# Performance work log

Measured on AMD Instinct MI355X. Metric: run time of the kernel, lower is better.

## Reference

```python
import jax, jax.numpy as jnp
import numpy as np

N_NODES = 50000
N_EDGES = 600000
D = 128
HIDDEN = 128
N_GRAPHS = 128
N_CLASSES = 10
N_STACKED = 3  # num_layers - 1


def setup_inputs() -> dict:
    key = jax.random.key(0)
    ks = jax.random.split(key, 12)
    s = 1.0 / np.sqrt(HIDDEN)
    inp = {
        "x": jax.random.normal(ks[0], (N_NODES, D), dtype=jnp.float32),
        "edge_index": jax.random.randint(ks[1], (2, N_EDGES), 0, N_NODES, dtype=jnp.int64),
        "batch": jnp.sort(jax.random.randint(ks[2], (N_NODES,), 0, N_GRAPHS, dtype=jnp.int64)),
        "W1": jax.random.normal(ks[3], (D, HIDDEN), dtype=jnp.float32) * s,
        "R1": jax.random.normal(ks[4], (D, HIDDEN), dtype=jnp.float32) * s,
        "b1": jnp.zeros((HIDDEN,), dtype=jnp.float32),
        "Wc": jax.random.normal(ks[5], (N_STACKED, HIDDEN, HIDDEN), dtype=jnp.float32) * s,
        "Rc": jax.random.normal(ks[6], (N_STACKED, HIDDEN, HIDDEN), dtype=jnp.float32) * s,
        "bc": jnp.zeros((N_STACKED, HIDDEN), dtype=jnp.float32),
        "lin1_w": jax.random.normal(ks[7], (HIDDEN, HIDDEN), dtype=jnp.float32) * s,
        "lin1_b": jnp.zeros((HIDDEN,), dtype=jnp.float32),
        "lin2_w": jax.random.normal(ks[8], (HIDDEN, N_CLASSES), dtype=jnp.float32) * s,
        "lin2_b": jnp.zeros((N_CLASSES,), dtype=jnp.float32),
    }
    return inp


def _gcn_norm(edge_index, n_nodes):
    # symmetric GCN normalization coeffs per edge (edge_weight=None -> ones)
    src, dst = edge_index[0], edge_index[1]
    ones = jnp.ones((edge_index.shape[1],), dtype=jnp.float32)
    deg = jax.ops.segment_sum(ones, dst, num_segments=n_nodes)
    dinv = jnp.where(deg > 0, jax.lax.rsqrt(jnp.maximum(deg, 1.0)), 0.0)
    return dinv[src] * dinv[dst]


def _gcs(x, src, dst, norm, W, R, b):
    # GCN aggregation on transformed features + linear skip (root) connection
    h = x @ W                                   # [N, H]
    msg = h[src] * norm[:, None]                # gather + scale, [E, H]
    agg = jax.ops.segment_sum(msg, dst, num_segments=x.shape[0])
    return agg + x @ R + b


def reference(x, edge_index, batch, W1, R1, b1, Wc, Rc, bc,
              lin1_w, lin1_b, lin2_w, lin2_b):
    src, dst = edge_index[0], edge_index[1]
    norm = _gcn_norm(edge_index, x.shape[0])

    h = jax.nn.relu(_gcs(x, src, dst, norm, W1, R1, b1))
    for i in range(N_STACKED):
        h = jax.nn.relu(_gcs(h, src, dst, norm, Wc[i], Rc[i], bc[i]))
    last = h

    # global mean pool over graphs
    sums = jax.ops.segment_sum(h, batch, num_segments=N_GRAPHS)
    cnts = jax.ops.segment_sum(jnp.ones((h.shape[0],), h.dtype), batch,
                               num_segments=N_GRAPHS)
    pooled = sums / jnp.maximum(cnts, 1.0)[:, None]

    g = jax.nn.relu(pooled @ lin1_w + lin1_b)   # dropout is identity in eval mode
    logits = g @ lin2_w + lin2_b
    return jax.nn.log_softmax(logits, axis=-1), last
```

## Files before the change

kernel.cpp:

```cpp
#include <hip/hip_runtime.h>

#define N_NODES  50000
#define N_EDGES  600000
#define DIM      128
#define N_GRAPHS 128
#define N_CLASSES 10
#define NB_SCAN  196
#define ZWORDS   1700000
#define NZB4     1661


typedef __bf16 bf16x8 __attribute__((ext_vector_type(8)));
typedef float  f32x4  __attribute__((ext_vector_type(4)));

__device__ inline unsigned short f2bf(float f) {
  union { float f; unsigned int i; } u; u.f = f;
  unsigned int r = u.i + 0x7fff + ((u.i >> 16) & 1);
  return (unsigned short)(r >> 16);
}
__device__ inline float bf2f(unsigned short s) {
  union { unsigned int i; float f; } u; u.i = ((unsigned int)s) << 16;
  return u.f;
}
__device__ inline bf16x8 pack8(float4 lo, float4 hi) {
  union { bf16x8 v; unsigned short s[8]; } u;
  u.s[0] = f2bf(lo.x); u.s[1] = f2bf(lo.y); u.s[2] = f2bf(lo.z); u.s[3] = f2bf(lo.w);
  u.s[4] = f2bf(hi.x); u.s[5] = f2bf(hi.y); u.s[6] = f2bf(hi.z); u.s[7] = f2bf(hi.w);
  return u.v;
}
__device__ inline bf16x8 zero8() {
  union { bf16x8 v; unsigned short s[8]; } u;
#pragma unroll
  for (int j = 0; j < 8; ++j) u.s[j] = 0;
  return u.v;
}


__global__ __launch_bounds__(256) void k_prep(float4* __restrict__ z4,
                                              const float* __restrict__ W1,
                                              const float* __restrict__ R1,
                                              const float* __restrict__ Wc,
                                              const float* __restrict__ Rc,
                                              unsigned short* __restrict__ pk) {
  if (blockIdx.x < NZB4) {
    int i = blockIdx.x * 256 + threadIdx.x;
    if (i < ZWORDS / 4) z4[i] = make_float4(0.f, 0.f, 0.f, 0.f);
    return;
  }
  int pb = blockIdx.x - NZB4;
  int mm = pb >> 3, sub = pb & 7;
  const float* src = (mm == 0) ? W1
                   : (mm < 4)  ? Wc + (size_t)(mm - 1) * DIM * DIM
                   : (mm == 4) ? R1
                               : Rc + (size_t)(mm - 5) * DIM * DIM;
  int idx = sub * 256 + threadIdx.x;
  int lane = idx & 63;
  int kc   = (idx >> 6) & 3;
  int nt   = idx >> 8;
  int col  = nt * 16 + (lane & 15);
  int k0   = kc * 32 + (lane >> 4) * 8;
  unsigned short* dst = pk + (size_t)mm * 16384 + (size_t)idx * 8;
  ushort4 u;
  u.x = f2bf(src[(k0 + 0) * DIM + col]);
  u.y = f2bf(src[(k0 + 1) * DIM + col]);
  u.z = f2bf(src[(k0 + 2) * DIM + col]);
  u.w = f2bf(src[(k0 + 3) * DIM + col]);
  *(ushort4*)&dst[0] = u;
  u.x = f2bf(src[(k0 + 4) * DIM + col]);
  u.y = f2bf(src[(k0 + 5) * DIM + col]);
  u.z = f2bf(src[(k0 + 6) * DIM + col]);
  u.w = f2bf(src[(k0 + 7) * DIM + col]);
  *(ushort4*)&dst[4] = u;
}


__global__ __launch_bounds__(256) void k_deg(const int* __restrict__ ei,
                                             int* __restrict__ deg) {
  int e = blockIdx.x * 256 + threadIdx.x;
  if (e < N_EDGES) atomicAdd(&deg[ei[N_EDGES + e]], 1);
}

__global__ __launch_bounds__(256) void k_dinvsum(const int* __restrict__ deg,
                                                 float* __restrict__ dinv,
                                                 int* __restrict__ bsum) {
  int i = blockIdx.x * 256 + threadIdx.x;
  int t = threadIdx.x;
  int d = (i < N_NODES) ? deg[i] : 0;
  if (i < N_NODES) dinv[i] = (d > 0) ? rsqrtf((float)d) : 0.f;
  int dp = (d + 7) & ~7;
  __shared__ int tmp[256];
  tmp[t] = dp;
  __syncthreads();
  for (int off = 128; off > 0; off >>= 1) {
    if (t < off) tmp[t] += tmp[t + off];
    __syncthreads();
  }
  if (t == 0) bsum[blockIdx.x] = tmp[0];
}

__global__ __launch_bounds__(256) void k_bscan(const int* __restrict__ bsum,
                                               int* __restrict__ boff,
                                               int* __restrict__ rowp) {
  int t = threadIdx.x;
  int v = (t < NB_SCAN) ? bsum[t] : 0;
  __shared__ int tmp[256];
  tmp[t] = v;
  __syncthreads();
  for (int off = 1; off < 256; off <<= 1) {
    int add = (t >= off) ? tmp[t - off] : 0;
    __syncthreads();
    tmp[t] += add;
    __syncthreads();
  }
  boff[t] = tmp[t] - v;
  if (t == 255) rowp[N_NODES] = tmp[255];
}

__global__ __launch_bounds__(256) void k_rowp(const int* __restrict__ deg,
                                              const int* __restrict__ boff,
                                              int* __restrict__ rowp) {
  int i = blockIdx.x * 256 + threadIdx.x;
  int t = threadIdx.x;
  int dp = (i < N_NODES) ? ((deg[i] + 7) & ~7) : 0;
  __shared__ int tmp[256];
  tmp[t] = dp;
  __syncthreads();
  for (int off = 1; off < 256; off <<= 1) {
    int add = (t >= off) ? tmp[t - off] : 0;
    __syncthreads();
    tmp[t] += add;
    __syncthreads();
  }
  if (i < N_NODES) rowp[i] = boff[blockIdx.x] + tmp[t] - dp;
}

__global__ __launch_bounds__(256) void k_fill(const int* __restrict__ ei,
                                              const int* __restrict__ rowp,
                                              int* __restrict__ cnt,
                                              const float* __restrict__ dinv,
                                              int2* __restrict__ epk) {
  int e = blockIdx.x * 256 + threadIdx.x;
  if (e < N_EDGES) {
    int s = ei[e];
    int d = ei[N_EDGES + e];
    int p = rowp[d] + atomicAdd(&cnt[d], 1);
    epk[p] = make_int2(s, __float_as_int(dinv[s] * dinv[d]));
  }
}


__global__ __launch_bounds__(256) void k_gemm0(const float* __restrict__ xf,
                                               const unsigned short* __restrict__ pkW,
                                               const unsigned short* __restrict__ pkR,
                                               const float* __restrict__ bv,
                                               unsigned short* __restrict__ hwb,
                                               unsigned short* __restrict__ skipb) {
  const int tid  = threadIdx.x;
  const int wave = tid >> 6, lane = tid & 63;
  const int m = lane & 15, q = lane >> 4;
  const int rbase = blockIdx.x * 64 + wave * 16;
  const int arow  = rbase + m;
  const bool aok  = arow < N_NODES;

  bf16x8 a[4];
#pragma unroll
  for (int kc = 0; kc < 4; ++kc) {
    float4 lo = make_float4(0.f, 0.f, 0.f, 0.f);
    float4 hi = make_float4(0.f, 0.f, 0.f, 0.f);
    if (aok) {
      lo = *(const float4*)&xf[arow * DIM + kc * 32 + q * 8];
      hi = *(const float4*)&xf[arow * DIM + kc * 32 + q * 8 + 4];
    }
    a[kc] = pack8(lo, hi);
  }

  f32x4 acc[16];
#pragma unroll
  for (int t = 0; t < 16; ++t) acc[t] = (f32x4){0.f, 0.f, 0.f, 0.f};

#pragma unroll
  for (int nt = 0; nt < 8; ++nt) {
    const unsigned short* pw = pkW + ((size_t)(nt * 4) * 64 + lane) * 8;
    const unsigned short* pr = pkR + ((size_t)(nt * 4) * 64 + lane) * 8;
#pragma unroll
    for (int kc = 0; kc < 4; ++kc) {
      bf16x8 bW = *(const bf16x8*)(pw + (size_t)kc * 64 * 8);
      acc[nt] = __builtin_amdgcn_mfma_f32_16x16x32_bf16(a[kc], bW, acc[nt], 0, 0, 0);
    }
#pragma unroll
    for (int kc = 0; kc < 4; ++kc) {
      bf16x8 bR = *(const bf16x8*)(pr + (size_t)kc * 64 * 8);
      acc[8 + nt] = __builtin_amdgcn_mfma_f32_16x16x32_bf16(a[kc], bR, acc[8 + nt], 0, 0, 0);
    }
  }

#pragma unroll
  for (int nt = 0; nt < 8; ++nt) {
    int col = nt * 16 + m;
    float bias = bv[col];
#pragma unroll
    for (int rg = 0; rg < 4; ++rg) {
      int row = rbase + q * 4 + rg;
      if (row < N_NODES) {
        hwb[row * DIM + col]   = f2bf(acc[nt][rg]);
        skipb[row * DIM + col] = f2bf(acc[8 + nt][rg] + bias);
      }
    }
  }
}


__global__ __launch_bounds__(256) void k_gath(const unsigned short* __restrict__ hin,
                                              const int* __restrict__ rowp,
                                              const int2* __restrict__ epk,
                                              const unsigned short* __restrict__ skipb,
                                              unsigned short* __restrict__ gout) {
  int n = blockIdx.x * 8 + (threadIdx.x >> 5);
  if (n >= N_NODES) return;
  int l4 = (threadIdx.x & 31) * 4;
  int e0 = rowp[n], e1 = rowp[n + 1];
  ushort4 s = *(const ushort4*)&skipb[n * DIM + l4];
  float4 accA = make_float4(0.f, 0.f, 0.f, 0.f);
  float4 accB = make_float4(0.f, 0.f, 0.f, 0.f);
  for (int ea = e0, eb = e1 - 4; ea < eb; ea += 4, eb -= 4) {
    int4 p0 = *(const int4*)&epk[ea];
    int4 p1 = *(const int4*)&epk[ea + 2];
    int4 p2 = *(const int4*)&epk[eb];
    int4 p3 = *(const int4*)&epk[eb + 2];
    ushort4 u0 = *(const ushort4*)&hin[p0.x * DIM + l4];
    ushort4 u1 = *(const ushort4*)&hin[p0.z * DIM + l4];
    ushort4 u2 = *(const ushort4*)&hin[p1.x * DIM + l4];
    ushort4 u3 = *(const ushort4*)&hin[p1.z * DIM + l4];
    ushort4 u4 = *(const ushort4*)&hin[p2.x * DIM + l4];
    ushort4 u5 = *(const ushort4*)&hin[p2.z * DIM + l4];
    ushort4 u6 = *(const ushort4*)&hin[p3.x * DIM + l4];
    ushort4 u7 = *(const ushort4*)&hin[p3.z * DIM + l4];
    float w0 = __int_as_float(p0.y), w1 = __int_as_float(p0.w);
    float w2 = __int_as_float(p1.y), w3 = __int_as_float(p1.w);
    float w4 = __int_as_float(p2.y), w5 = __int_as_float(p2.w);
    float w6 = __int_as_float(p3.y), w7 = __int_as_float(p3.w);
    accA.x = fmaf(w0, bf2f(u0.x), fmaf(w1, bf2f(u1.x), fmaf(w2, bf2f(u2.x), fmaf(w3, bf2f(u3.x), accA.x))));
    accA.y = fmaf(w0, bf2f(u0.y), fmaf(w1, bf2f(u1.y), fmaf(w2, bf2f(u2.y), fmaf(w3, bf2f(u3.y), accA.y))));
    accA.z = fmaf(w0, bf2f(u0.z), fmaf(w1, bf2f(u1.z), fmaf(w2, bf2f(u2.z), fmaf(w3, bf2f(u3.z), accA.z))));
    accA.w = fmaf(w0, bf2f(u0.w), fmaf(w1, bf2f(u1.w), fmaf(w2, bf2f(u2.w), fmaf(w3, bf2f(u3.w), accA.w))));
    accB.x = fmaf(w4, bf2f(u4.x), fmaf(w5, bf2f(u5.x), fmaf(w6, bf2f(u6.x), fmaf(w7, bf2f(u7.x), accB.x))));
    accB.y = fmaf(w4, bf2f(u4.y), fmaf(w5, bf2f(u5.y), fmaf(w6, bf2f(u6.y), fmaf(w7, bf2f(u7.y), accB.y))));
    accB.z = fmaf(w4, bf2f(u4.z), fmaf(w5, bf2f(u5.z), fmaf(w6, bf2f(u6.z), fmaf(w7, bf2f(u7.z), accB.z))));
    accB.w = fmaf(w4, bf2f(u4.w), fmaf(w5, bf2f(u5.w), fmaf(w6, bf2f(u6.w), fmaf(w7, bf2f(u7.w), accB.w))));
  }
  ushort4 o;
  o.x = f2bf(fmaxf(accA.x + accB.x + bf2f(s.x), 0.f));
  o.y = f2bf(fmaxf(accA.y + accB.y + bf2f(s.y), 0.f));
  o.z = f2bf(fmaxf(accA.z + accB.z + bf2f(s.z), 0.f));
  o.w = f2bf(fmaxf(accA.w + accB.w + bf2f(s.w), 0.f));
  *(ushort4*)&gout[n * DIM + l4] = o;
}


template<bool LAST>
__global__ __launch_bounds__(256) void k_gemmb(unsigned short* __restrict__ gio,
                                               const unsigned short* __restrict__ pkW,
                                               const unsigned short* __restrict__ pkR,
                                               const float* __restrict__ bv,
                                               unsigned short* __restrict__ skipb,
                                               float* __restrict__ skipf) {
  const int tid  = threadIdx.x;
  const int wave = tid >> 6, lane = tid & 63;
  const int m = lane & 15, q = lane >> 4;
  const int rbase = blockIdx.x * 64 + wave * 16;
  const int arow  = rbase + m;
  const bool aok  = arow < N_NODES;

  bf16x8 a[4];
#pragma unroll
  for (int kc = 0; kc < 4; ++kc)
    a[kc] = aok ? *(const bf16x8*)&gio[arow * DIM + kc * 32 + q * 8] : zero8();

  f32x4 acc[16];
#pragma unroll
  for (int t = 0; t < 16; ++t) acc[t] = (f32x4){0.f, 0.f, 0.f, 0.f};

#pragma unroll
  for (int nt = 0; nt < 8; ++nt) {
    const unsigned short* pw = pkW + ((size_t)(nt * 4) * 64 + lane) * 8;
    const unsigned short* pr = pkR + ((size_t)(nt * 4) * 64 + lane) * 8;
#pragma unroll
    for (int kc = 0; kc < 4; ++kc) {
      bf16x8 bW = *(const bf16x8*)(pw + (size_t)kc * 64 * 8);
      acc[nt] = __builtin_amdgcn_mfma_f32_16x16x32_bf16(a[kc], bW, acc[nt], 0, 0, 0);
    }
#pragma unroll
    for (int kc = 0; kc < 4; ++kc) {
      bf16x8 bR = *(const bf16x8*)(pr + (size_t)kc * 64 * 8);
      acc[8 + nt] = __builtin_amdgcn_mfma_f32_16x16x32_bf16(a[kc], bR, acc[8 + nt], 0, 0, 0);
    }
  }

#pragma unroll
  for (int nt = 0; nt < 8; ++nt) {
    int col = nt * 16 + m;
    float bias = bv[col];
#pragma unroll
    for (int rg = 0; rg < 4; ++rg) {
      int row = rbase + q * 4 + rg;
      if (row < N_NODES) {
        gio[row * DIM + col] = f2bf(acc[nt][rg]);
        float v = acc[8 + nt][rg] + bias;
        if (LAST) skipf[row * DIM + col] = v;
        else      skipb[row * DIM + col] = f2bf(v);
      }
    }
  }
}


__global__ __launch_bounds__(256) void k_aggF(const unsigned short* __restrict__ hwb,
                                              const int* __restrict__ rowp,
                                              const int2* __restrict__ epk,
                                              float* __restrict__ actf) {
  int n = blockIdx.x * 8 + (threadIdx.x >> 5);
  if (n >= N_NODES) return;
  int l4 = (threadIdx.x & 31) * 4;
  int e0 = rowp[n], e1 = rowp[n + 1];
  float4 s = *(const float4*)&actf[n * DIM + l4];
  float4 accA = make_float4(0.f, 0.f, 0.f, 0.f);
  float4 accB = make_float4(0.f, 0.f, 0.f, 0.f);
  for (int ea = e0, eb = e1 - 4; ea < eb; ea += 4, eb -= 4) {
    int4 p0 = *(const int4*)&epk[ea];
    int4 p1 = *(const int4*)&epk[ea + 2];
    int4 p2 = *(const int4*)&epk[eb];
    int4 p3 = *(const int4*)&epk[eb + 2];
    ushort4 u0 = *(const ushort4*)&hwb[p0.x * DIM + l4];
    ushort4 u1 = *(const ushort4*)&hwb[p0.z * DIM + l4];
    ushort4 u2 = *(const ushort4*)&hwb[p1.x * DIM + l4];
    ushort4 u3 = *(const ushort4*)&hwb[p1.z * DIM + l4];
    ushort4 u4 = *(const ushort4*)&hwb[p2.x * DIM + l4];
    ushort4 u5 = *(const ushort4*)&hwb[p2.z * DIM + l4];
    ushort4 u6 = *(const ushort4*)&hwb[p3.x * DIM + l4];
    ushort4 u7 = *(const ushort4*)&hwb[p3.z * DIM + l4];
    float w0 = __int_as_float(p0.y), w1 = __int_as_float(p0.w);
    float w2 = __int_as_float(p1.y), w3 = __int_as_float(p1.w);
    float w4 = __int_as_float(p2.y), w5 = __int_as_float(p2.w);
    float w6 = __int_as_float(p3.y), w7 = __int_as_float(p3.w);
    accA.x = fmaf(w0, bf2f(u0.x), fmaf(w1, bf2f(u1.x), fmaf(w2, bf2f(u2.x), fmaf(w3, bf2f(u3.x), accA.x))));
    accA.y = fmaf(w0, bf2f(u0.y), fmaf(w1, bf2f(u1.y), fmaf(w2, bf2f(u2.y), fmaf(w3, bf2f(u3.y), accA.y))));
    accA.z = fmaf(w0, bf2f(u0.z), fmaf(w1, bf2f(u1.z), fmaf(w2, bf2f(u2.z), fmaf(w3, bf2f(u3.z), accA.z))));
    accA.w = fmaf(w0, bf2f(u0.w), fmaf(w1, bf2f(u1.w), fmaf(w2, bf2f(u2.w), fmaf(w3, bf2f(u3.w), accA.w))));
    accB.x = fmaf(w4, bf2f(u4.x), fmaf(w5, bf2f(u5.x), fmaf(w6, bf2f(u6.x), fmaf(w7, bf2f(u7.x), accB.x))));
    accB.y = fmaf(w4, bf2f(u4.y), fmaf(w5, bf2f(u5.y), fmaf(w6, bf2f(u6.y), fmaf(w7, bf2f(u7.y), accB.y))));
    accB.z = fmaf(w4, bf2f(u4.z), fmaf(w5, bf2f(u5.z), fmaf(w6, bf2f(u6.z), fmaf(w7, bf2f(u7.z), accB.z))));
    accB.w = fmaf(w4, bf2f(u4.w), fmaf(w5, bf2f(u5.w), fmaf(w6, bf2f(u6.w), fmaf(w7, bf2f(u7.w), accB.w))));
  }
  float4 o;
  o.x = fmaxf(accA.x + accB.x + s.x, 0.f);
  o.y = fmaxf(accA.y + accB.y + s.y, 0.f);
  o.z = fmaxf(accA.z + accB.z + s.z, 0.f);
  o.w = fmaxf(accA.w + accB.w + s.w, 0.f);
  *(float4*)&actf[n * DIM + l4] = o;
}


__global__ __launch_bounds__(1024) void k_pool2(const float* __restrict__ h,
                                                const int* __restrict__ batch,
                                                float* __restrict__ pooled) {
  int g = blockIdx.x;
  int t = threadIdx.x;
  __shared__ int sb[2];
  if (t < 2) {
    int target = g + t;
    int lo = 0, hi = N_NODES;
    while (lo < hi) {
      int mid = (lo + hi) >> 1;
      if (batch[mid] < target) lo = mid + 1; else hi = mid;
    }
    sb[t] = lo;
  }
  __syncthreads();
  int start = sb[0], end = sb[1];
  int c = t & 127, rg = t >> 7;
  float acc = 0.f;
  for (int r = start + rg; r < end; r += 8) acc += h[r * DIM + c];
  __shared__ float sp[8][DIM];
  sp[rg][c] = acc;
  __syncthreads();
  if (rg == 0) {
    float tot = acc;
#pragma unroll
    for (int i = 1; i < 8; ++i) tot += sp[i][c];
    float cnt = fmaxf((float)(end - start), 1.f);
    pooled[g * DIM + c] = tot / cnt;
  }
}


__global__ __launch_bounds__(128) void k_mlp1(const float* __restrict__ pooled,
                                              const float* __restrict__ w,
                                              const float* __restrict__ bias,
                                              float* __restrict__ g1) {
  int g = blockIdx.x, t = threadIdx.x;
  __shared__ float sp[DIM];
  sp[t] = pooled[g * DIM + t];
  __syncthreads();
  float acc = bias[t];
#pragma unroll 4
  for (int k = 0; k < DIM; ++k) acc = fmaf(sp[k], w[k * DIM + t], acc);
  g1[g * DIM + t] = fmaxf(acc, 0.f);
}

__global__ __launch_bounds__(128) void k_mlp2(const float* __restrict__ g1,
                                              const float* __restrict__ w,
                                              const float* __restrict__ bias,
                                              float* __restrict__ out) {
  int g = threadIdx.x;
  float l[N_CLASSES];
#pragma unroll
  for (int c = 0; c < N_CLASSES; ++c) l[c] = bias[c];
  for (int k = 0; k < DIM; ++k) {
    float gv = g1[g * DIM + k];
#pragma unroll
    for (int c = 0; c < N_CLASSES; ++c) l[c] = fmaf(gv, w[k * N_CLASSES + c], l[c]);
  }
  float m = l[0];
#pragma unroll
  for (int c = 1; c < N_CLASSES; ++c) m = fmaxf(m, l[c]);
  float s = 0.f;
#pragma unroll
  for (int c = 0; c < N_CLASSES; ++c) s += expf(l[c] - m);
  float lse = logf(s) + m;
#pragma unroll
  for (int c = 0; c < N_CLASSES; ++c) out[g * N_CLASSES + c] = l[c] - lse;
}


extern "C" void kernel_launch(void* const* d_in, const int* in_sizes, int n_in,
                              void* d_out, int out_size, void* d_ws, size_t ws_size,
                              hipStream_t stream) {
  const float* x     = (const float*)d_in[0];
  const int* ei      = (const int*)d_in[1];
  const int* batch   = (const int*)d_in[2];
  const float* W1  = (const float*)d_in[3];
  const float* R1  = (const float*)d_in[4];
  const float* b1  = (const float*)d_in[5];
  const float* Wc  = (const float*)d_in[6];
  const float* Rc  = (const float*)d_in[7];
  const float* bc  = (const float*)d_in[8];
  const float* l1w = (const float*)d_in[9];
  const float* l1b = (const float*)d_in[10];
  const float* l2w = (const float*)d_in[11];
  const float* l2b = (const float*)d_in[12];

  float* out   = (float*)d_out;
  float* dlast = out + N_GRAPHS * N_CLASSES;

  float* ws = (float*)d_ws;
  unsigned short* X = (unsigned short*)ws;
  unsigned short* Y = (unsigned short*)(ws + 3203072);
  unsigned short* S = (unsigned short*)(ws + 6406144);
  int*   deg   = (int*)(ws + 9609216);
  int*   cnt   = (int*)(ws + 9659216);
  int2*  epk   = (int2*)(ws + 9709216);
  float* dinv  = ws + 11309216;
  int*   rowp  = (int*)(ws + 11359216);
  float* pooled= ws + 11409232;
  float* g1    = ws + 11425616;
  unsigned short* pk = (unsigned short*)(ws + 11442000);
  int*   bsum  = (int*)(ws + 11507536);
  int*   boff  = (int*)(ws + 11507792);

  k_prep<<<NZB4 + 64, 256, 0, stream>>>((float4*)(ws + 9609216), W1, R1, Wc, Rc, pk);
  k_deg <<<(N_EDGES + 255) / 256, 256, 0, stream>>>(ei, deg);
  k_dinvsum<<<NB_SCAN, 256, 0, stream>>>(deg, dinv, bsum);
  k_bscan<<<1, 256, 0, stream>>>(bsum, boff, rowp);
  k_rowp<<<NB_SCAN, 256, 0, stream>>>(deg, boff, rowp);
  k_fill<<<(N_EDGES + 255) / 256, 256, 0, stream>>>(ei, rowp, cnt, dinv, epk);

  const int NGB = (N_NODES + 63) / 64;
  const int NAB = (N_NODES + 7) / 8;

  k_gemm0<<<NGB, 256, 0, stream>>>(x, pk + 0 * 16384, pk + 4 * 16384, b1, X, S);
  k_gath <<<NAB, 256, 0, stream>>>(X, rowp, epk, S, Y);
  k_gemmb<false><<<NGB, 256, 0, stream>>>(Y, pk + 1 * 16384, pk + 5 * 16384,
                                          bc + 0 * DIM, S, nullptr);
  k_gath <<<NAB, 256, 0, stream>>>(Y, rowp, epk, S, X);
  k_gemmb<false><<<NGB, 256, 0, stream>>>(X, pk + 2 * 16384, pk + 6 * 16384,
                                          bc + 1 * DIM, S, nullptr);
  k_gath <<<NAB, 256, 0, stream>>>(X, rowp, epk, S, Y);
  k_gemmb<true><<<NGB, 256, 0, stream>>>(Y, pk + 3 * 16384, pk + 7 * 16384,
                                         bc + 2 * DIM, S, dlast);
  k_aggF<<<NAB, 256, 0, stream>>>(Y, rowp, epk, dlast);

  k_pool2<<<N_GRAPHS, 1024, 0, stream>>>(dlast, batch, pooled);
  k_mlp1<<<N_GRAPHS, 128, 0, stream>>>(pooled, l1w, l1b, g1);
  k_mlp2<<<1, N_GRAPHS, 0, stream>>>(g1, l2w, l2b, out);
}
```

Baseline: 386.0 us.

## Fuse mean-pool into final aggregation, stage GEMM stores via LDS, add nontemporal hints

The last aggregation kernel now accumulates per-graph partial sums in shared memory and adds them to a zeroed psum buffer with atomics. This removes the separate pooling kernel and its re-read of the final fp32 activations, and mlp1 divides by the graph node counts. The GEMM epilogues stage bf16 outputs through LDS so each row is written with 16-byte stores instead of scattered 2-byte ones. Many streaming loads and stores in the gather and aggregation kernels are marked nontemporal. The costs are extra atomics, more LDS use per GEMM block, and possible cache side effects from the nontemporal hints.

```diff
diff --git a/kernel.cpp b/kernel.cpp
--- a/kernel.cpp
+++ b/kernel.cpp
@@ -8,10 +8,14 @@
 #define NB_SCAN  196
 #define ZWORDS   1700000
 #define NZB4     1661
+#define NPB      16
 
 
 typedef __bf16 bf16x8 __attribute__((ext_vector_type(8)));
 typedef float  f32x4  __attribute__((ext_vector_type(4)));
+typedef int    i32x4  __attribute__((ext_vector_type(4)));
+typedef unsigned short u16x4 __attribute__((ext_vector_type(4)));
+typedef unsigned short u16x8 __attribute__((ext_vector_type(8)));
 
 __device__ inline unsigned short f2bf(float f) {
   union { float f; unsigned int i; } u; u.f = f;
@@ -37,6 +41,7 @@
 
 
 __global__ __launch_bounds__(256) void k_prep(float4* __restrict__ z4,
+                                              float4* __restrict__ pz,
                                               const float* __restrict__ W1,
                                               const float* __restrict__ R1,
                                               const float* __restrict__ Wc,
@@ -47,7 +52,12 @@
     if (i < ZWORDS / 4) z4[i] = make_float4(0.f, 0.f, 0.f, 0.f);
     return;
   }
-  int pb = blockIdx.x - NZB4;
+  if (blockIdx.x < NZB4 + NPB) {
+    int i = (blockIdx.x - NZB4) * 256 + threadIdx.x;
+    pz[i] = make_float4(0.f, 0.f, 0.f, 0.f);
+    return;
+  }
+  int pb = blockIdx.x - NZB4 - NPB;
   int mm = pb >> 3, sub = pb & 7;
   const float* src = (mm == 0) ? W1
                    : (mm < 4)  ? Wc + (size_t)(mm - 1) * DIM * DIM
@@ -155,6 +165,8 @@
                                                const float* __restrict__ bv,
                                                unsigned short* __restrict__ hwb,
                                                unsigned short* __restrict__ skipb) {
+  __shared__ unsigned short eh[4][16 * 136];
+  __shared__ unsigned short es[4][16 * 136];
   const int tid  = threadIdx.x;
   const int wave = tid >> 6, lane = tid & 63;
   const int m = lane & 15, q = lane >> 4;
@@ -196,15 +208,25 @@
 
 #pragma unroll
   for (int nt = 0; nt < 8; ++nt) {
-    int col = nt * 16 + m;
-    float bias = bv[col];
+    float bias = bv[nt * 16 + m];
 #pragma unroll
     for (int rg = 0; rg < 4; ++rg) {
-      int row = rbase + q * 4 + rg;
-      if (row < N_NODES) {
-        hwb[row * DIM + col]   = f2bf(acc[nt][rg]);
-        skipb[row * DIM + col] = f2bf(acc[8 + nt][rg] + bias);
-      }
+      int r = q * 4 + rg;
+      eh[wave][r * 136 + nt * 16 + m] = f2bf(acc[nt][rg]);
+      es[wave][r * 136 + nt * 16 + m] = f2bf(acc[8 + nt][rg] + bias);
+    }
+  }
+  __syncthreads();
+#pragma unroll
+  for (int k = 0; k < 4; ++k) {
+    int c = k * 64 + lane;
+    int r = c >> 4, cb = c & 15;
+    int row = rbase + r;
+    u16x8 vh = *(const u16x8*)&eh[wave][r * 136 + cb * 8];
+    u16x8 vs = *(const u16x8*)&es[wave][r * 136 + cb * 8];
+    if (row < N_NODES) {
+      *(u16x8*)&hwb[row * DIM + cb * 8]   = vh;
+      *(u16x8*)&skipb[row * DIM + cb * 8] = vs;
     }
   }
 }
@@ -219,26 +241,26 @@
   if (n >= N_NODES) return;
   int l4 = (threadIdx.x & 31) * 4;
   int e0 = rowp[n], e1 = rowp[n + 1];
-  ushort4 s = *(const ushort4*)&skipb[n * DIM + l4];
+  u16x4 s = __builtin_nontemporal_load((const u16x4*)&skipb[n * DIM + l4]);
   float4 accA = make_float4(0.f, 0.f, 0.f, 0.f);
   float4 accB = make_float4(0.f, 0.f, 0.f, 0.f);
   for (int ea = e0, eb = e1 - 4; ea < eb; ea += 4, eb -= 4) {
-    int4 p0 = *(const int4*)&epk[ea];
-    int4 p1 = *(const int4*)&epk[ea + 2];
-    int4 p2 = *(const int4*)&epk[eb];
-    int4 p3 = *(const int4*)&epk[eb + 2];
-    ushort4 u0 = *(const ushort4*)&hin[p0.x * DIM + l4];
-    ushort4 u1 = *(const ushort4*)&hin[p0.z * DIM + l4];
-    ushort4 u2 = *(const ushort4*)&hin[p1.x * DIM + l4];
-    ushort4 u3 = *(const ushort4*)&hin[p1.z * DIM + l4];
-    ushort4 u4 = *(const ushort4*)&hin[p2.x * DIM + l4];
-    ushort4 u5 = *(const ushort4*)&hin[p2.z * DIM + l4];
-    ushort4 u6 = *(const ushort4*)&hin[p3.x * DIM + l4];
-    ushort4 u7 = *(const ushort4*)&hin[p3.z * DIM + l4];
-    float w0 = __int_as_float(p0.y), w1 = __int_as_float(p0.w);
-    float w2 = __int_as_float(p1.y), w3 = __int_as_float(p1.w);
-    float w4 = __int_as_float(p2.y), w5 = __int_as_float(p2.w);
-    float w6 = __int_as_float(p3.y), w7 = __int_as_float(p3.w);
+    i32x4 p0 = __builtin_nontemporal_load((const i32x4*)&epk[ea]);
+    i32x4 p1 = __builtin_nontemporal_load((const i32x4*)&epk[ea + 2]);
+    i32x4 p2 = __builtin_nontemporal_load((const i32x4*)&epk[eb]);
+    i32x4 p3 = __builtin_nontemporal_load((const i32x4*)&epk[eb + 2]);
+    ushort4 u0 = *(const ushort4*)&hin[p0[0] * DIM + l4];
+    ushort4 u1 = *(const ushort4*)&hin[p0[2] * DIM + l4];
+    ushort4 u2 = *(const ushort4*)&hin[p1[0] * DIM + l4];
+    ushort4 u3 = *(const ushort4*)&hin[p1[2] * DIM + l4];
+    ushort4 u4 = *(const ushort4*)&hin[p2[0] * DIM + l4];
+    ushort4 u5 = *(const ushort4*)&hin[p2[2] * DIM + l4];
+    ushort4 u6 = *(const ushort4*)&hin[p3[0] * DIM + l4];
+    ushort4 u7 = *(const ushort4*)&hin[p3[2] * DIM + l4];
+    float w0 = __int_as_float(p0[1]), w1 = __int_as_float(p0[3]);
+    float w2 = __int_as_float(p1[1]), w3 = __int_as_float(p1[3]);
+    float w4 = __int_as_float(p2[1]), w5 = __int_as_float(p2[3]);
+    float w6 = __int_as_float(p3[1]), w7 = __int_as_float(p3[3]);
     accA.x = fmaf(w0, bf2f(u0.x), fmaf(w1, bf2f(u1.x), fmaf(w2, bf2f(u2.x), fmaf(w3, bf2f(u3.x), accA.x))));
     accA.y = fmaf(w0, bf2f(u0.y), fmaf(w1, bf2f(u1.y), fmaf(w2, bf2f(u2.y), fmaf(w3, bf2f(u3.y), accA.y))));
     accA.z = fmaf(w0, bf2f(u0.z), fmaf(w1, bf2f(u1.z), fmaf(w2, bf2f(u2.z), fmaf(w3, bf2f(u3.z), accA.z))));
@@ -248,12 +270,12 @@
     accB.z = fmaf(w4, bf2f(u4.z), fmaf(w5, bf2f(u5.z), fmaf(w6, bf2f(u6.z), fmaf(w7, bf2f(u7.z), accB.z))));
     accB.w = fmaf(w4, bf2f(u4.w), fmaf(w5, bf2f(u5.w), fmaf(w6, bf2f(u6.w), fmaf(w7, bf2f(u7.w), accB.w))));
   }
-  ushort4 o;
-  o.x = f2bf(fmaxf(accA.x + accB.x + bf2f(s.x), 0.f));
-  o.y = f2bf(fmaxf(accA.y + accB.y + bf2f(s.y), 0.f));
-  o.z = f2bf(fmaxf(accA.z + accB.z + bf2f(s.z), 0.f));
-  o.w = f2bf(fmaxf(accA.w + accB.w + bf2f(s.w), 0.f));
-  *(ushort4*)&gout[n * DIM + l4] = o;
+  u16x4 o;
+  o[0] = f2bf(fmaxf(accA.x + accB.x + bf2f(s[0]), 0.f));
+  o[1] = f2bf(fmaxf(accA.y + accB.y + bf2f(s[1]), 0.f));
+  o[2] = f2bf(fmaxf(accA.z + accB.z + bf2f(s[2]), 0.f));
+  o[3] = f2bf(fmaxf(accA.w + accB.w + bf2f(s[3]), 0.f));
+  __builtin_nontemporal_store(o, (u16x4*)&gout[n * DIM + l4]);
 }
 
 
@@ -264,6 +286,8 @@
                                                const float* __restrict__ bv,
                                                unsigned short* __restrict__ skipb,
                                                float* __restrict__ skipf) {
+  __shared__ unsigned short eh[4][16 * 136];
+  __shared__ unsigned short es[4][16 * 136];
   const int tid  = threadIdx.x;
   const int wave = tid >> 6, lane = tid & 63;
   const int m = lane & 15, q = lane >> 4;
@@ -298,16 +322,39 @@
 
 #pragma unroll
   for (int nt = 0; nt < 8; ++nt) {
-    int col = nt * 16 + m;
-    float bias = bv[col];
+    float bias = bv[nt * 16 + m];
 #pragma unroll
     for (int rg = 0; rg < 4; ++rg) {
-      int row = rbase + q * 4 + rg;
-      if (row < N_NODES) {
-        gio[row * DIM + col] = f2bf(acc[nt][rg]);
-        float v = acc[8 + nt][rg] + bias;
-        if (LAST) skipf[row * DIM + col] = v;
-        else      skipb[row * DIM + col] = f2bf(v);
+      int r = q * 4 + rg;
+      eh[wave][r * 136 + nt * 16 + m] = f2bf(acc[nt][rg]);
+      if (!LAST) es[wave][r * 136 + nt * 16 + m] = f2bf(acc[8 + nt][rg] + bias);
+    }
+  }
+  if (LAST) {
+#pragma unroll
+    for (int nt = 0; nt < 8; ++nt) {
+      int col = nt * 16 + m;
+      float bias = bv[col];
+#pragma unroll
+      for (int rg = 0; rg < 4; ++rg) {
+        int row = rbase + q * 4 + rg;
+        if (row < N_NODES)
+          __builtin_nontemporal_store(acc[8 + nt][rg] + bias, &skipf[row * DIM + col]);
+      }
+    }
+  }
+  __syncthreads();
+#pragma unroll
+  for (int k = 0; k < 4; ++k) {
+    int c = k * 64 + lane;
+    int r = c >> 4, cb = c & 15;
+    int row = rbase + r;
+    u16x8 vh = *(const u16x8*)&eh[wave][r * 136 + cb * 8];
+    if (row < N_NODES) {
+      *(u16x8*)&gio[row * DIM + cb * 8] = vh;
+      if (!LAST) {
+        u16x8 vs = *(const u16x8*)&es[wave][r * 136 + cb * 8];
+        __builtin_nontemporal_store(vs, (u16x8*)&skipb[row * DIM + cb * 8]);
       }
     }
   }
@@ -317,31 +364,37 @@
 __global__ __launch_bounds__(256) void k_aggF(const unsigned short* __restrict__ hwb,
                                               const int* __restrict__ rowp,
                                               const int2* __restrict__ epk,
-                                              float* __restrict__ actf) {
-  int n = blockIdx.x * 8 + (threadIdx.x >> 5);
-  if (n >= N_NODES) return;
-  int l4 = (threadIdx.x & 31) * 4;
+                                              const int* __restrict__ batch,
+                                              float* __restrict__ actf,
+                                              float* __restrict__ psum) {
+  __shared__ float sp[8][132];
+  __shared__ int gb[8];
+  const int tid = threadIdx.x;
+  const int n0 = blockIdx.x * 8;
+  const int n = n0 + (tid >> 5);
+  const int l4 = (tid & 31) * 4;
+  if (tid < 8) gb[tid] = batch[n0 + tid];
   int e0 = rowp[n], e1 = rowp[n + 1];
-  float4 s = *(const float4*)&actf[n * DIM + l4];
+  f32x4 s = __builtin_nontemporal_load((const f32x4*)&actf[n * DIM + l4]);
   float4 accA = make_float4(0.f, 0.f, 0.f, 0.f);
   float4 accB = make_float4(0.f, 0.f, 0.f, 0.f);
   for (int ea = e0, eb = e1 - 4; ea < eb; ea += 4, eb -= 4) {
-    int4 p0 = *(const int4*)&epk[ea];
-    int4 p1 = *(const int4*)&epk[ea + 2];
-    int4 p2 = *(const int4*)&epk[eb];
-    int4 p3 = *(const int4*)&epk[eb + 2];
-    ushort4 u0 = *(const ushort4*)&hwb[p0.x * DIM + l4];
-    ushort4 u1 = *(const ushort4*)&hwb[p0.z * DIM + l4];
-    ushort4 u2 = *(const ushort4*)&hwb[p1.x * DIM + l4];
-    ushort4 u3 = *(const ushort4*)&hwb[p1.z * DIM + l4];
-    ushort4 u4 = *(const ushort4*)&hwb[p2.x * DIM + l4];
-    ushort4 u5 = *(const ushort4*)&hwb[p2.z * DIM + l4];
-    ushort4 u6 = *(const ushort4*)&hwb[p3.x * DIM + l4];
-    ushort4 u7 = *(const ushort4*)&hwb[p3.z * DIM + l4];
-    float w0 = __int_as_float(p0.y), w1 = __int_as_float(p0.w);
-    float w2 = __int_as_float(p1.y), w3 = __int_as_float(p1.w);
-    float w4 = __int_as_float(p2.y), w5 = __int_as_float(p2.w);
-    float w6 = __int_as_float(p3.y), w7 = __int_as_float(p3.w);
+    i32x4 p0 = __builtin_nontemporal_load((const i32x4*)&epk[ea]);
+    i32x4 p1 = __builtin_nontemporal_load((const i32x4*)&epk[ea + 2]);
+    i32x4 p2 = __builtin_nontemporal_load((const i32x4*)&epk[eb]);
+    i32x4 p3 = __builtin_nontemporal_load((const i32x4*)&epk[eb + 2]);
+    ushort4 u0 = *(const ushort4*)&hwb[p0[0] * DIM + l4];
+    ushort4 u1 = *(const ushort4*)&hwb[p0[2] * DIM + l4];
+    ushort4 u2 = *(const ushort4*)&hwb[p1[0] * DIM + l4];
+    ushort4 u3 = *(const ushort4*)&hwb[p1[2] * DIM + l4];
+    ushort4 u4 = *(const ushort4*)&hwb[p2[0] * DIM + l4];
+    ushort4 u5 = *(const ushort4*)&hwb[p2[2] * DIM + l4];
+    ushort4 u6 = *(const ushort4*)&hwb[p3[0] * DIM + l4];
+    ushort4 u7 = *(const ushort4*)&hwb[p3[2] * DIM + l4];
+    float w0 = __int_as_float(p0[1]), w1 = __int_as_float(p0[3]);
+    float w2 = __int_as_float(p1[1]), w3 = __int_as_float(p1[3]);
+    float w4 = __int_as_float(p2[1]), w5 = __int_as_float(p2[3]);
+    float w6 = __int_as_float(p3[1]), w7 = __int_as_float(p3[3]);
     accA.x = fmaf(w0, bf2f(u0.x), fmaf(w1, bf2f(u1.x), fmaf(w2, bf2f(u2.x), fmaf(w3, bf2f(u3.x), accA.x))));
     accA.y = fmaf(w0, bf2f(u0.y), fmaf(w1, bf2f(u1.y), fmaf(w2, bf2f(u2.y), fmaf(w3, bf2f(u3.y), accA.y))));
     accA.z = fmaf(w0, bf2f(u0.z), fmaf(w1, bf2f(u1.z), fmaf(w2, bf2f(u2.z), fmaf(w3, bf2f(u3.z), accA.z))));
@@ -351,20 +404,36 @@
     accB.z = fmaf(w4, bf2f(u4.z), fmaf(w5, bf2f(u5.z), fmaf(w6, bf2f(u6.z), fmaf(w7, bf2f(u7.z), accB.z))));
     accB.w = fmaf(w4, bf2f(u4.w), fmaf(w5, bf2f(u5.w), fmaf(w6, bf2f(u6.w), fmaf(w7, bf2f(u7.w), accB.w))));
   }
-  float4 o;
-  o.x = fmaxf(accA.x + accB.x + s.x, 0.f);
-  o.y = fmaxf(accA.y + accB.y + s.y, 0.f);
-  o.z = fmaxf(accA.z + accB.z + s.z, 0.f);
-  o.w = fmaxf(accA.w + accB.w + s.w, 0.f);
-  *(float4*)&actf[n * DIM + l4] = o;
-}
-
-
-__global__ __launch_bounds__(1024) void k_pool2(const float* __restrict__ h,
-                                                const int* __restrict__ batch,
-                                                float* __restrict__ pooled) {
-  int g = blockIdx.x;
-  int t = threadIdx.x;
+  f32x4 o;
+  o[0] = fmaxf(accA.x + accB.x + s[0], 0.f);
+  o[1] = fmaxf(accA.y + accB.y + s[1], 0.f);
+  o[2] = fmaxf(accA.z + accB.z + s[2], 0.f);
+  o[3] = fmaxf(accA.w + accB.w + s[3], 0.f);
+  __builtin_nontemporal_store(o, (f32x4*)&actf[n * DIM + l4]);
+  int r = tid >> 5;
+  sp[r][l4 + 0] = o[0]; sp[r][l4 + 1] = o[1];
+  sp[r][l4 + 2] = o[2]; sp[r][l4 + 3] = o[3];
+  __syncthreads();
+  if (tid < DIM) {
+    int gprev = gb[0];
+    float acc = 0.f;
+#pragma unroll
+    for (int rr = 0; rr < 8; ++rr) {
+      int g = gb[rr];
+      if (g != gprev) { atomicAdd(&psum[gprev * DIM + tid], acc); acc = 0.f; gprev = g; }
+      acc += sp[rr][tid];
+    }
+    atomicAdd(&psum[gprev * DIM + tid], acc);
+  }
+}
+
+
+__global__ __launch_bounds__(128) void k_mlp1(const float* __restrict__ psum,
+                                              const int* __restrict__ batch,
+                                              const float* __restrict__ w,
+                                              const float* __restrict__ bias,
+                                              float* __restrict__ g1) {
+  int g = blockIdx.x, t = threadIdx.x;
   __shared__ int sb[2];
   if (t < 2) {
     int target = g + t;
@@ -376,30 +445,9 @@
     sb[t] = lo;
   }
   __syncthreads();
-  int start = sb[0], end = sb[1];
-  int c = t & 127, rg = t >> 7;
-  float acc = 0.f;
-  for (int r = start + rg; r < end; r += 8) acc += h[r * DIM + c];
-  __shared__ float sp[8][DIM];
-  sp[rg][c] = acc;
-  __syncthreads();
-  if (rg == 0) {
-    float tot = acc;
-#pragma unroll
-    for (int i = 1; i < 8; ++i) tot += sp[i][c];
-    float cnt = fmaxf((float)(end - start), 1.f);
-    pooled[g * DIM + c] = tot / cnt;
-  }
-}
-
-
-__global__ __launch_bounds__(128) void k_mlp1(const float* __restrict__ pooled,
-                                              const float* __restrict__ w,
-                                              const float* __restrict__ bias,
-                                              float* __restrict__ g1) {
-  int g = blockIdx.x, t = threadIdx.x;
+  float cnt = fmaxf((float)(sb[1] - sb[0]), 1.f);
   __shared__ float sp[DIM];
-  sp[t] = pooled[g * DIM + t];
+  sp[t] = psum[g * DIM + t] / cnt;
   __syncthreads();
   float acc = bias[t];
 #pragma unroll 4
@@ -461,13 +509,14 @@
   int2*  epk   = (int2*)(ws + 9709216);
   float* dinv  = ws + 11309216;
   int*   rowp  = (int*)(ws + 11359216);
-  float* pooled= ws + 11409232;
+  float* psum  = ws + 11409232;
   float* g1    = ws + 11425616;
   unsigned short* pk = (unsigned short*)(ws + 11442000);
   int*   bsum  = (int*)(ws + 11507536);
   int*   boff  = (int*)(ws + 11507792);
 
-  k_prep<<<NZB4 + 64, 256, 0, stream>>>((float4*)(ws + 9609216), W1, R1, Wc, Rc, pk);
+  k_prep<<<NZB4 + NPB + 64, 256, 0, stream>>>((float4*)(ws + 9609216),
+                                              (float4*)psum, W1, R1, Wc, Rc, pk);
   k_deg <<<(N_EDGES + 255) / 256, 256, 0, stream>>>(ei, deg);
   k_dinvsum<<<NB_SCAN, 256, 0, stream>>>(deg, dinv, bsum);
   k_bscan<<<1, 256, 0, stream>>>(bsum, boff, rowp);
@@ -487,9 +536,8 @@
   k_gath <<<NAB, 256, 0, stream>>>(X, rowp, epk, S, Y);
   k_gemmb<true><<<NGB, 256, 0, stream>>>(Y, pk + 3 * 16384, pk + 7 * 16384,
                                          bc + 2 * DIM, S, dlast);
-  k_aggF<<<NAB, 256, 0, stream>>>(Y, rowp, epk, dlast);
-
-  k_pool2<<<N_GRAPHS, 1024, 0, stream>>>(dlast, batch, pooled);
-  k_mlp1<<<N_GRAPHS, 128, 0, stream>>>(pooled, l1w, l1b, g1);
+  k_aggF<<<NAB, 256, 0, stream>>>(Y, rowp, epk, batch, dlast, psum);
+
+  k_mlp1<<<N_GRAPHS, 128, 0, stream>>>(psum, batch, l1w, l1b, g1);
   k_mlp2<<<1, N_GRAPHS, 0, stream>>>(g1, l2w, l2b, out);
 }
```

After: 418.8 us. 1.09x slower.
